# Kernel tuning notes

Hardware: AMD Instinct MI355X
Metric: run time of the kernel (lower is better)

The kernel has to match this reference:

```python
import jax, jax.numpy as jnp
import numpy as np

L = 50
RHO = 1.0

def _get_index():
    # S = {(m,n) | |mn| <= rho*L//2, |m|<=L/2, |n|<=L/2, n >= |m|}  (index_type 'A')
    S = []
    for m in range(-L // 2, L // 2 + 1):
        for n in range(-L // 2, L // 2 + 1):
            if abs(m * n) <= RHO * L // 2 and n >= abs(m):
                S.append((m, n))
    return np.asarray(S, dtype=np.int32)  # [S, 2], S = 118 for rho=1, L=50


def setup_inputs() -> dict:
    key = jax.random.key(0)
    k1, k2 = jax.random.split(key)
    B, W, M = 2, 16384, 2  # batch, window length, dual-pol modes
    E_real = jax.random.normal(k1, (B, W, M), dtype=jnp.float32)
    E_imag = jax.random.normal(k2, (B, W, M), dtype=jnp.float32)
    return {"E_real": E_real, "E_imag": E_imag}


def _roll_many(E, shifts):
    # torch.roll(E, s, dims=-2) for every s in shifts, vectorized.
    # E: [B, W, M], shifts: [S] -> [B, S, W, M]
    W = E.shape[1]
    idx = (jnp.arange(W)[None, :] - shifts[:, None]) % W  # [S, W]
    return E[:, idx, :]


def _triple(Xa, Xb, Xc):
    # (Xa * conj(Xb) + pol-swap) * Xc  -- the dual-pol (Nmodes=2) term
    A = Xa * jnp.conj(Xb)
    return (A + jnp.roll(A, 1, axis=-1)) * Xc


def _features(E):
    # E: [B, W, M] complex64 -> F: [B, W, M, S] complex64
    idx = _get_index()
    m = jnp.asarray(idx[:, 0])
    n = jnp.asarray(idx[:, 1])
    Rm = _roll_many(E, m)            # roll by m
    Rn = _roll_many(E, n)            # roll by n
    Rmn = _roll_many(E, m + n)       # roll by m+n
    R_m = _roll_many(E, -m)
    R_n = _roll_many(E, -n)
    R_mn = _roll_many(E, -(m + n))
    # Emn + Emn_  (two-term value for generic (m,n))
    T1 = _triple(Rn, Rmn, Rm) + _triple(R_n, R_mn, R_m)
    # Enm + Enm_  (role-swapped terms, added only when n > |m|)
    T2 = _triple(Rm, Rmn, Rn) + _triple(R_m, R_mn, R_n)
    # m=n=0: original computes a single term = T1/2; n>|m|: T1+T2; else (n==|m|, m!=0): T1
    w1 = jnp.where((m == 0) & (n == 0), 0.5, 1.0).astype(jnp.float32)[None, :, None, None]
    w2 = jnp.where(n > jnp.abs(m), 1.0, 0.0).astype(jnp.float32)[None, :, None, None]
    F = w1 * T1 + w2 * T2            # [B, S, W, M]
    return jnp.transpose(F, (0, 2, 3, 1))  # [B, W, M, S]


def reference(E_real, E_imag):
    E = jax.lax.complex(E_real, E_imag)  # complex64
    F = _features(E)
    # split complex output into trailing real/imag channel for a real-valued baseline
    return jnp.stack([jnp.real(F), jnp.imag(F)], axis=-1)  # [B, W, M, S, 2]
```

## Files before the change

kernel.cpp:

```cpp
#include <hip/hip_runtime.h>


constexpr int W = 16384;
constexpr int WMASK = W - 1;
constexpr int NB = 2;
constexpr int S = 118;
constexpr int HALO = 26;
constexpr int TILE_W = 16;
constexpr int LDSW = TILE_W + 2 * HALO;

struct C2 { float re, im; };

__device__ inline void decode_s(int s, int& m, int& n) {
    const int g = (s>=1)+(s>=4)+(s>=10)+(s>=21)+(s>=46)
                + (s>=72)+(s>=97)+(s>=108)+(s>=114)+(s>=117);
    const int start = (s>=117)?117:(s>=114)?114:(s>=108)?108:(s>=97)?97:
                      (s>=72)?72:(s>=46)?46:(s>=21)?21:(s>=10)?10:
                      (s>=4)?4:(s>=1)?1:0;
    m = g - 5;
    const int am = (m < 0) ? -m : m;
    n = am + (s - start);
}

__device__ inline C2 bracket(const float4 a, const float4 b) {
    C2 r;
    r.re = a.x*b.x + a.y*b.y + a.z*b.z + a.w*b.w;
    r.im = a.y*b.x - a.x*b.y + a.w*b.z - a.z*b.w;
    return r;
}

__device__ inline float4 compute_f(const float4 Am, const float4 Ap,
                                   const float4 An, const float4 Bn,
                                   const float4 Amn, const float4 Bmn,
                                   const float w1, const float w2) {
    const C2 B1 = bracket(An, Amn);
    const C2 B2 = bracket(Bn, Bmn);
    float r0 = B1.re*Am.x - B1.im*Am.y + B2.re*Ap.x - B2.im*Ap.y;
    float i0 = B1.re*Am.y + B1.im*Am.x + B2.re*Ap.y + B2.im*Ap.x;
    float r1 = B1.re*Am.z - B1.im*Am.w + B2.re*Ap.z - B2.im*Ap.w;
    float i1 = B1.re*Am.w + B1.im*Am.z + B2.re*Ap.w + B2.im*Ap.z;
    r0 *= w1; i0 *= w1; r1 *= w1; i1 *= w1;
    C2 B3 = bracket(Am, Amn);
    C2 B4 = bracket(Ap, Bmn);
    B3.re *= w2; B3.im *= w2; B4.re *= w2; B4.im *= w2;
    r0 += B3.re*An.x - B3.im*An.y + B4.re*Bn.x - B4.im*Bn.y;
    i0 += B3.re*An.y + B3.im*An.x + B4.re*Bn.y + B4.im*Bn.x;
    r1 += B3.re*An.z - B3.im*An.w + B4.re*Bn.z - B4.im*Bn.w;
    i1 += B3.re*An.w + B3.im*An.z + B4.re*Bn.w + B4.im*Bn.z;
    return make_float4(r0, i0, r1, i1);
}

__global__ __launch_bounds__(256) void sympbc_kernel(
    const float* __restrict__ Er, const float* __restrict__ Ei,
    float* __restrict__ out)
{
    __shared__ float4 lds[LDSW];

    const int tid = threadIdx.x;
    const int b = blockIdx.y;
    const int tile0 = blockIdx.x * TILE_W;

    if (tid < LDSW) {
        const int gw = (tile0 - HALO + tid) & WMASK;
        const size_t gi = ((size_t)b * W + gw) * 2;
        const float2 r = *reinterpret_cast<const float2*>(Er + gi);
        const float2 i = *reinterpret_cast<const float2*>(Ei + gi);
        lds[tid] = make_float4(r.x, i.x, r.y, i.y);
    }
    __syncthreads();

    const int sp = tid & 63;
    const int wsub = tid >> 6;
    if (sp >= 59) return;

    const int s0 = 2 * sp;
    int m0, n0, m1, n1;
    decode_s(s0, m0, n0);
    decode_s(s0 + 1, m1, n1);
    const int am0 = (m0 < 0) ? -m0 : m0;
    const int am1 = (m1 < 0) ? -m1 : m1;
    const float w1a = (s0 == 46) ? 0.5f : 1.0f;
    const float w2a = (n0 > am0) ? 1.0f : 0.0f;
    const float w2b = (n1 > am1) ? 1.0f : 0.0f;
    const bool mdiff = (m1 != m0);

    float* obase = out + ((size_t)b * W + tile0) * (2 * S * 2) + (size_t)s0 * 2;

    #pragma unroll
    for (int it = 0; it < TILE_W / 4; ++it) {
        const int wl = wsub + 4 * it;
        const int ci = HALO + wl;

        const float4 Am = lds[ci - m0];
        const float4 Ap = lds[ci + m0];
        float4 Am1v = Am, Ap1v = Ap;
        if (mdiff) { Am1v = lds[ci - m1]; Ap1v = lds[ci + m1]; }

        const float4 An0  = lds[ci - n0];
        const float4 Bn0  = lds[ci + n0];
        const float4 Amn0 = lds[ci - m0 - n0];
        const float4 Bmn0 = lds[ci + m0 + n0];
        const float4 An1  = lds[ci - n1];
        const float4 Bn1  = lds[ci + n1];
        const float4 Amn1 = lds[ci - m1 - n1];
        const float4 Bmn1 = lds[ci + m1 + n1];

        const float4 F0 = compute_f(Am,   Ap,   An0, Bn0, Amn0, Bmn0, w1a, w2a);
        const float4 F1 = compute_f(Am1v, Ap1v, An1, Bn1, Amn1, Bmn1, 1.0f, w2b);

        float* orow = obase + (size_t)wl * (2 * S * 2);
        *reinterpret_cast<float4*>(orow) =
            make_float4(F0.x, F0.y, F1.x, F1.y);
        *reinterpret_cast<float4*>(orow + S * 2) =
            make_float4(F0.z, F0.w, F1.z, F1.w);
    }
}

extern "C" void kernel_launch(void* const* d_in, const int* in_sizes, int n_in,
                              void* d_out, int out_size, void* d_ws, size_t ws_size,
                              hipStream_t stream) {
    const float* Er = (const float*)d_in[0];
    const float* Ei = (const float*)d_in[1];
    float* out = (float*)d_out;
    dim3 grid(W / TILE_W, NB);
    sympbc_kernel<<<grid, dim3(256), 0, stream>>>(Er, Ei, out);
}
```

Measured before the change: 20.17 us.

## Stage output through swizzled LDS buffer and widen tile to 64 positions

Raises the tile to 64 window positions and changes the thread mapping so each lane handles one position while the waves walk feature indices in chunks of 32. Results go into an XOR-swizzled shared-memory buffer and are then written back with threads mapped along the feature dimension. The aim is more contiguous global stores and a smaller halo overhead per tile. In exchange it adds two barriers per chunk, uses more LDS, and now issues float2 stores instead of float4 stores.

```diff
diff --git a/kernel.cpp b/kernel.cpp
--- a/kernel.cpp
+++ b/kernel.cpp
@@ -6,8 +6,9 @@
 constexpr int NB = 2;
 constexpr int S = 118;
 constexpr int HALO = 26;
-constexpr int TILE_W = 16;
+constexpr int TILE_W = 64;
 constexpr int LDSW = TILE_W + 2 * HALO;
+constexpr int CHUNK = 32;
 
 struct C2 { float re, im; };
 
@@ -54,7 +55,8 @@
     const float* __restrict__ Er, const float* __restrict__ Ei,
     float* __restrict__ out)
 {
-    __shared__ float4 lds[LDSW];
+    __shared__ float4 eld[LDSW];
+    __shared__ float4 obuf[CHUNK][TILE_W];
 
     const int tid = threadIdx.x;
     const int b = blockIdx.y;
@@ -65,54 +67,60 @@
         const size_t gi = ((size_t)b * W + gw) * 2;
         const float2 r = *reinterpret_cast<const float2*>(Er + gi);
         const float2 i = *reinterpret_cast<const float2*>(Ei + gi);
-        lds[tid] = make_float4(r.x, i.x, r.y, i.y);
+        eld[tid] = make_float4(r.x, i.x, r.y, i.y);
     }
     __syncthreads();
 
-    const int sp = tid & 63;
-    const int wsub = tid >> 6;
-    if (sp >= 59) return;
+    const int lane = tid & 63;
+    const int wv   = tid >> 6;
+    const int ci   = HALO + lane;
 
-    const int s0 = 2 * sp;
-    int m0, n0, m1, n1;
-    decode_s(s0, m0, n0);
-    decode_s(s0 + 1, m1, n1);
-    const int am0 = (m0 < 0) ? -m0 : m0;
-    const int am1 = (m1 < 0) ? -m1 : m1;
-    const float w1a = (s0 == 46) ? 0.5f : 1.0f;
-    const float w2a = (n0 > am0) ? 1.0f : 0.0f;
-    const float w2b = (n1 > am1) ? 1.0f : 0.0f;
-    const bool mdiff = (m1 != m0);
+    const int s2    = tid & 31;
+    const int wbase = tid >> 5;
 
-    float* obase = out + ((size_t)b * W + tile0) * (2 * S * 2) + (size_t)s0 * 2;
+    const size_t orow0 = ((size_t)b * W + tile0) * 472;
 
     #pragma unroll
-    for (int it = 0; it < TILE_W / 4; ++it) {
-        const int wl = wsub + 4 * it;
-        const int ci = HALO + wl;
+    for (int chunk = 0; chunk < (S + CHUNK - 1) / CHUNK; ++chunk) {
+        const int s_lo = chunk * CHUNK;
+        const int s_n  = (S - s_lo < CHUNK) ? (S - s_lo) : CHUNK;
 
-        const float4 Am = lds[ci - m0];
-        const float4 Ap = lds[ci + m0];
-        float4 Am1v = Am, Ap1v = Ap;
-        if (mdiff) { Am1v = lds[ci - m1]; Ap1v = lds[ci + m1]; }
+        #pragma unroll
+        for (int k = 0; k < CHUNK / 4; ++k) {
+            const int sl = wv + 4 * k;
+            if (sl < s_n) {
+                const int s = s_lo + sl;
+                int m, n;
+                decode_s(s, m, n);
+                const int am = (m < 0) ? -m : m;
+                const float w1 = (s == 46) ? 0.5f : 1.0f;
+                const float w2 = (n > am) ? 1.0f : 0.0f;
 
-        const float4 An0  = lds[ci - n0];
-        const float4 Bn0  = lds[ci + n0];
-        const float4 Amn0 = lds[ci - m0 - n0];
-        const float4 Bmn0 = lds[ci + m0 + n0];
-        const float4 An1  = lds[ci - n1];
-        const float4 Bn1  = lds[ci + n1];
-        const float4 Amn1 = lds[ci - m1 - n1];
-        const float4 Bmn1 = lds[ci + m1 + n1];
+                const float4 Am  = eld[ci - m];
+                const float4 Ap  = eld[ci + m];
+                const float4 An  = eld[ci - n];
+                const float4 Bn  = eld[ci + n];
+                const float4 Amn = eld[ci - m - n];
+                const float4 Bmn = eld[ci + m + n];
 
-        const float4 F0 = compute_f(Am,   Ap,   An0, Bn0, Amn0, Bmn0, w1a, w2a);
-        const float4 F1 = compute_f(Am1v, Ap1v, An1, Bn1, Amn1, Bmn1, 1.0f, w2b);
+                obuf[sl][lane ^ (sl & 7)] =
+                    compute_f(Am, Ap, An, Bn, Amn, Bmn, w1, w2);
+            }
+        }
+        __syncthreads();
 
-        float* orow = obase + (size_t)wl * (2 * S * 2);
-        *reinterpret_cast<float4*>(orow) =
-            make_float4(F0.x, F0.y, F1.x, F1.y);
-        *reinterpret_cast<float4*>(orow + S * 2) =
-            make_float4(F0.z, F0.w, F1.z, F1.w);
+        if (s2 < s_n) {
+            const size_t scol = (size_t)(s_lo + s2) * 2;
+            #pragma unroll
+            for (int j = 0; j < TILE_W / 8; ++j) {
+                const int w = j * 8 + wbase;
+                const float4 F = obuf[s2][w ^ (s2 & 7)];
+                float* o = out + orow0 + (size_t)w * 472 + scol;
+                *reinterpret_cast<float2*>(o)       = make_float2(F.x, F.y);
+                *reinterpret_cast<float2*>(o + 236) = make_float2(F.z, F.w);
+            }
+        }
+        __syncthreads();
     }
 }
 
```

Measured after the change: 24.04 us. 1.19x slower.
